# Kernel optimization log

Measured on AMD Instinct MI355X. Metric: run time of the kernel, lower is better.

## Reference

```python
import jax, jax.numpy as jnp
import numpy as np

B, S, D = 4, 2048, 1024
H = 16
HD = D // H  # head_dim = 64


def setup_inputs() -> dict:
    key = jax.random.key(0)
    ks = jax.random.split(key, 5)
    scale = 1.0 / np.sqrt(D)
    return {
        "sequence_features": jax.random.normal(ks[0], (B, S, D), dtype=jnp.float32),
        "Wq": jax.random.normal(ks[1], (D, D), dtype=jnp.float32) * scale,
        "bq": jnp.zeros((D,), dtype=jnp.float32),
        "Wk": jax.random.normal(ks[2], (D, D), dtype=jnp.float32) * scale,
        "bk": jnp.zeros((D,), dtype=jnp.float32),
        "Wv": jax.random.normal(ks[3], (D, D), dtype=jnp.float32) * scale,
        "bv": jnp.zeros((D,), dtype=jnp.float32),
        "Wo": jax.random.normal(ks[4], (D, D), dtype=jnp.float32) * scale,
        "bo": jnp.zeros((D,), dtype=jnp.float32),
    }


def reference(sequence_features, Wq, bq, Wk, bk, Wv, bv, Wo, bo):
    x = sequence_features  # [B, S, D]
    # projections (torch Linear: x @ W.T + b; here W stored as [D_in, D_out])
    Q = x @ Wq + bq
    K = x @ Wk + bk
    V = x @ Wv + bv
    # split heads -> [B, H, S, HD]
    def heads(t):
        return t.reshape(B, S, H, HD).transpose(0, 2, 1, 3)
    Qh, Kh, Vh = heads(Q), heads(K), heads(V)
    # scaled dot-product attention (no mask, dropout off / eval mode)
    energy = jnp.einsum("bhqd,bhkd->bhqk", Qh, Kh) / jnp.sqrt(jnp.float32(HD))
    attn = jax.nn.softmax(energy, axis=-1)
    ctx = jnp.einsum("bhqk,bhkd->bhqd", attn, Vh)  # [B, H, S, HD]
    ctx = ctx.transpose(0, 2, 1, 3).reshape(B, S, D)
    out = ctx @ Wo + bo  # [B, S, D]
    return out.mean(axis=1)  # context vector [B, D]
```

## Files before the change

kernel.cpp:

```cpp
#include <hip/hip_runtime.h>
#include <hip/hip_bf16.h>

#define NB 4
#define NS 2048
#define ND 1024
#define NH 16

typedef __attribute__((ext_vector_type(8))) short short8;
typedef __attribute__((ext_vector_type(4))) float f32x4;

__device__ __forceinline__ unsigned short f2b(float f) {
  unsigned int u = __float_as_uint(f);
  u = (u + 0x7fffu + ((u >> 16) & 1u)) >> 16;
  return (unsigned short)u;
}
__device__ __forceinline__ unsigned int pkbf(float a, float b) {
  return (unsigned int)f2b(a) | ((unsigned int)f2b(b) << 16);
}
__device__ __forceinline__ void gload16(const void* g, void* l) {
  __builtin_amdgcn_global_load_lds(
      (const __attribute__((address_space(1))) unsigned int*)g,
      (__attribute__((address_space(3))) unsigned int*)l, 16, 0, 0);
}
__device__ __forceinline__ int sw2(int row) { return (row ^ (row >> 2)) & 3; }

__global__ void conv_x(const float* __restrict__ x, unsigned short* __restrict__ xb) {
  int i = blockIdx.x * 256 + threadIdx.x;
  float4 v = ((const float4*)x)[i];
  ushort4 o;
  o.x = f2b(v.x); o.y = f2b(v.y); o.z = f2b(v.z); o.w = f2b(v.w);
  ((ushort4*)xb)[i] = o;
}

__global__ void conv_wt(const float* __restrict__ Wq, const float* __restrict__ Wk,
                        const float* __restrict__ Wv, unsigned short* __restrict__ Wtq,
                        unsigned short* __restrict__ Wtk, unsigned short* __restrict__ Wtv) {
  const int z = blockIdx.z;
  const float* W = (z == 0) ? Wq : (z == 1) ? Wk : Wv;
  unsigned short* Wt = (z == 0) ? Wtq : (z == 1) ? Wtk : Wtv;
  __shared__ float t[32][33];
  const int tid = threadIdx.x;
  const int row = tid >> 3, c4 = (tid & 7) * 4;
  float4 v = *(const float4*)(W + (size_t)(blockIdx.y * 32 + row) * ND + blockIdx.x * 32 + c4);
  t[row][c4] = v.x; t[row][c4 + 1] = v.y; t[row][c4 + 2] = v.z; t[row][c4 + 3] = v.w;
  __syncthreads();
  ushort4 o;
  o.x = f2b(t[c4][row]); o.y = f2b(t[c4 + 1][row]);
  o.z = f2b(t[c4 + 2][row]); o.w = f2b(t[c4 + 3][row]);
  *(ushort4*)(Wt + (size_t)(blockIdx.x * 32 + row) * ND + blockIdx.y * 32 + c4) = o;
}

__global__ __launch_bounds__(256) void qkv_gemm(
    const unsigned short* __restrict__ xb,
    const unsigned short* __restrict__ Wtq, const unsigned short* __restrict__ Wtk,
    const unsigned short* __restrict__ Wtv,
    const float* __restrict__ bq, const float* __restrict__ bk, const float* __restrict__ bv,
    unsigned short* __restrict__ Qb, unsigned short* __restrict__ Kb,
    unsigned short* __restrict__ Vt) {
  const int z = blockIdx.z;
  const unsigned short* Wt = (z == 0) ? Wtq : (z == 1) ? Wtk : Wtv;
  const float* bias = (z == 0) ? bq : (z == 1) ? bk : bv;
  const int tn = blockIdx.x, tm = blockIdx.y;
  __shared__ __align__(16) unsigned short Al[2][128 * 32];
  __shared__ __align__(16) unsigned short Bl[2][128 * 32];
  const int tid = threadIdx.x;
  const int lane = tid & 63, w = tid >> 6;
  const int c = lane & 15, g = lane >> 4;
  const int mo = (w >> 1) * 64, no = (w & 1) * 64;

  f32x4 acc[4][4];
#pragma unroll
  for (int i = 0; i < 4; i++)
#pragma unroll
    for (int j = 0; j < 4; j++) acc[i][j] = (f32x4){0.f, 0.f, 0.f, 0.f};

  const int r0 = tid >> 2, g0 = tid & 3;
  const int r1 = (256 + tid) >> 2, g1 = (256 + tid) & 3;
  const unsigned short* gA0 = xb + (size_t)(tm * 128 + r0) * ND + (g0 ^ sw2(r0)) * 8;
  const unsigned short* gA1 = xb + (size_t)(tm * 128 + r1) * ND + (g1 ^ sw2(r1)) * 8;
  const unsigned short* gB0 = Wt + (size_t)(tn * 128 + r0) * ND + (g0 ^ sw2(r0)) * 8;
  const unsigned short* gB1 = Wt + (size_t)(tn * 128 + r1) * ND + (g1 ^ sw2(r1)) * 8;
  const int lo0 = w * 512, lo1 = 2048 + w * 512;

  gload16(gA0, &Al[0][lo0]); gload16(gA1, &Al[0][lo1]);
  gload16(gB0, &Bl[0][lo0]); gload16(gB1, &Bl[0][lo1]);
  __syncthreads();

  for (int kk = 0; kk < 32; ++kk) {
    const int cur = kk & 1;
    if (kk < 31) {
      const int ko = (kk + 1) * 32;
      gload16(gA0 + ko, &Al[cur ^ 1][lo0]); gload16(gA1 + ko, &Al[cur ^ 1][lo1]);
      gload16(gB0 + ko, &Bl[cur ^ 1][lo0]); gload16(gB1 + ko, &Bl[cur ^ 1][lo1]);
    }
    short8 af[4], bf[4];
#pragma unroll
    for (int i = 0; i < 4; i++) {
      int row = mo + i * 16 + c;
      af[i] = *(const short8*)&Al[cur][row * 32 + (g ^ sw2(row)) * 8];
    }
#pragma unroll
    for (int j = 0; j < 4; j++) {
      int row = no + j * 16 + c;
      bf[j] = *(const short8*)&Bl[cur][row * 32 + (g ^ sw2(row)) * 8];
    }
#pragma unroll
    for (int i = 0; i < 4; i++)
#pragma unroll
      for (int j = 0; j < 4; j++)
        acc[i][j] = __builtin_amdgcn_mfma_f32_16x16x32_bf16(af[i], bf[j], acc[i][j], 0, 0, 0);
    __syncthreads();
  }

  if (z < 2) {
    unsigned short* Out = (z == 0) ? Qb : Kb;
    const float sc = (z == 0) ? 0.125f : 1.0f;
#pragma unroll
    for (int j = 0; j < 4; j++) {
      int col = tn * 128 + no + j * 16 + c;
      float bv_ = bias[col];
#pragma unroll
      for (int i = 0; i < 4; i++) {
        int rowb = tm * 128 + mo + i * 16 + 4 * g;
#pragma unroll
        for (int r = 0; r < 4; r++) {
          float v = (acc[i][j][r] + bv_) * sc;
          float vn = __shfl_xor(v, 1, 64);
          if (!(lane & 1))
            *(unsigned int*)(Out + (size_t)(rowb + r) * ND + col) = pkbf(v, vn);
        }
      }
    }
  } else {
#pragma unroll
    for (int j = 0; j < 4; j++) {
      int col = tn * 128 + no + j * 16 + c;
      float bv_ = bias[col];
      int h = col >> 6, hd = col & 63;
#pragma unroll
      for (int i = 0; i < 4; i++) {
        int rowg = tm * 128 + mo + i * 16 + 4 * g;
        int bi = rowg >> 11, s = rowg & 2047;
        uint2 u;
        u.x = pkbf(acc[i][j][0] + bv_, acc[i][j][1] + bv_);
        u.y = pkbf(acc[i][j][2] + bv_, acc[i][j][3] + bv_);
        *(uint2*)(Vt + ((size_t)((bi * NH + h) * 64 + hd) * NS + s)) = u;
      }
    }
  }
}

__global__ __launch_bounds__(256) void attn_kernel(
    const unsigned short* __restrict__ Qb, const unsigned short* __restrict__ Kb,
    const unsigned short* __restrict__ Vt, float* __restrict__ mean_ctx) {
  const int qt = blockIdx.x, h = blockIdx.y, b = blockIdx.z;
  const int tid = threadIdx.x, lane = tid & 63, w = tid >> 6;
  const int c = lane & 15, g = lane >> 4;
  __shared__ __align__(16) unsigned short Klds[2][32 * 64];
  __shared__ __align__(16) unsigned short Vlds[2][64 * 32];
  __shared__ float redl[4][64];

  const int qg = qt * 64 + w * 16 + c;
  const unsigned short* qbase = Qb + (size_t)(b * NS + qg) * ND + h * 64 + g * 8;
  const short8 qf0 = *(const short8*)(qbase);
  const short8 qf1 = *(const short8*)(qbase + 32);

  const int krow = tid >> 3, kg = tid & 7;
  const unsigned short* gK = Kb + (size_t)(b * NS + krow) * ND + h * 64 + ((kg ^ (krow & 7)) * 8);
  const int vd = tid >> 2, vg = tid & 3;
  const unsigned short* gV = Vt + (size_t)((b * NH + h) * 64 + vd) * NS + ((vg ^ sw2(vd)) * 8);

  f32x4 accc[4];
#pragma unroll
  for (int nt = 0; nt < 4; nt++) accc[nt] = (f32x4){0.f, 0.f, 0.f, 0.f};
  float m_run = -1e30f, l_run = 0.f;

  gload16(gK, &Klds[0][w * 512]);
  gload16(gV, &Vlds[0][w * 512]);
  __syncthreads();

  for (int kc = 0; kc < 64; ++kc) {
    const int cur = kc & 1;
    if (kc < 63) {
      gload16(gK + (size_t)(kc + 1) * 32 * ND, &Klds[cur ^ 1][w * 512]);
      gload16(gV + (kc + 1) * 32, &Vlds[cur ^ 1][w * 512]);
    }
    f32x4 accE[2];
#pragma unroll
    for (int mt = 0; mt < 2; ++mt) {
      int row = mt * 16 + c;
      short8 k0 = *(const short8*)&Klds[cur][row * 64 + ((g ^ (row & 7)) * 8)];
      short8 k1 = *(const short8*)&Klds[cur][row * 64 + (((g + 4) ^ (row & 7)) * 8)];
      f32x4 zz = (f32x4){0.f, 0.f, 0.f, 0.f};
      accE[mt] = __builtin_amdgcn_mfma_f32_16x16x32_bf16(k0, qf0, zz, 0, 0, 0);
      accE[mt] = __builtin_amdgcn_mfma_f32_16x16x32_bf16(k1, qf1, accE[mt], 0, 0, 0);
    }
    float cm = fmaxf(fmaxf(fmaxf(accE[0][0], accE[0][1]), fmaxf(accE[0][2], accE[0][3])),
                     fmaxf(fmaxf(accE[1][0], accE[1][1]), fmaxf(accE[1][2], accE[1][3])));
    cm = fmaxf(cm, __shfl_xor(cm, 16, 64));
    cm = fmaxf(cm, __shfl_xor(cm, 32, 64));
    float mnew = fmaxf(m_run, cm);
    float sf = __expf(m_run - mnew);
    float p[8];
#pragma unroll
    for (int r = 0; r < 4; r++) {
      p[r] = __expf(accE[0][r] - mnew);
      p[4 + r] = __expf(accE[1][r] - mnew);
    }
    float cs = ((p[0] + p[1]) + (p[2] + p[3])) + ((p[4] + p[5]) + (p[6] + p[7]));
    cs += __shfl_xor(cs, 16, 64);
    cs += __shfl_xor(cs, 32, 64);
    l_run = l_run * sf + cs;
    m_run = mnew;
    float sf0 = __shfl(sf, 4 * g + 0, 64), sf1 = __shfl(sf, 4 * g + 1, 64);
    float sf2 = __shfl(sf, 4 * g + 2, 64), sf3 = __shfl(sf, 4 * g + 3, 64);
#pragma unroll
    for (int nt = 0; nt < 4; nt++) {
      accc[nt][0] *= sf0; accc[nt][1] *= sf1; accc[nt][2] *= sf2; accc[nt][3] *= sf3;
    }
    unsigned int pk0 = pkbf(p[0], p[1]), pk1 = pkbf(p[2], p[3]);
    unsigned int pk2 = pkbf(p[4], p[5]), pk3 = pkbf(p[6], p[7]);
    int srcA = (g & 1) * 32 + c, srcB = srcA + 16;
    unsigned int a0 = (unsigned int)__shfl((int)pk0, srcA, 64);
    unsigned int h0 = (unsigned int)__shfl((int)pk2, srcA, 64);
    unsigned int a1 = (unsigned int)__shfl((int)pk1, srcA, 64);
    unsigned int h1 = (unsigned int)__shfl((int)pk3, srcA, 64);
    unsigned int a2 = (unsigned int)__shfl((int)pk0, srcB, 64);
    unsigned int h2 = (unsigned int)__shfl((int)pk2, srcB, 64);
    unsigned int a3 = (unsigned int)__shfl((int)pk1, srcB, 64);
    unsigned int h3 = (unsigned int)__shfl((int)pk3, srcB, 64);
    union { unsigned int u[4]; short8 v; } pf;
    pf.u[0] = (g < 2) ? a0 : h0;
    pf.u[1] = (g < 2) ? a1 : h1;
    pf.u[2] = (g < 2) ? a2 : h2;
    pf.u[3] = (g < 2) ? a3 : h3;
#pragma unroll
    for (int nt = 0; nt < 4; nt++) {
      int d = nt * 16 + c;
      short8 vf = *(const short8*)&Vlds[cur][d * 32 + ((g ^ sw2(d)) * 8)];
      accc[nt] = __builtin_amdgcn_mfma_f32_16x16x32_bf16(pf.v, vf, accc[nt], 0, 0, 0);
    }
    __syncthreads();
  }

  float i0 = 1.f / __shfl(l_run, 4 * g + 0, 64);
  float i1 = 1.f / __shfl(l_run, 4 * g + 1, 64);
  float i2 = 1.f / __shfl(l_run, 4 * g + 2, 64);
  float i3 = 1.f / __shfl(l_run, 4 * g + 3, 64);
#pragma unroll
  for (int nt = 0; nt < 4; nt++) {
    float s = accc[nt][0] * i0 + accc[nt][1] * i1 + accc[nt][2] * i2 + accc[nt][3] * i3;
    s += __shfl_xor(s, 16, 64);
    s += __shfl_xor(s, 32, 64);
    if (g == 0) redl[w][nt * 16 + c] = s;
  }
  __syncthreads();
  if (tid < 64) {
    float tot = redl[0][tid] + redl[1][tid] + redl[2][tid] + redl[3][tid];
    atomicAdd(&mean_ctx[(size_t)b * ND + h * 64 + tid], tot * (1.0f / (float)NS));
  }
}

__global__ void out_proj(const float* __restrict__ mc, const float* __restrict__ Wo,
                         const float* __restrict__ bo, float* __restrict__ out) {
  const int b = blockIdx.y;
  const int d = blockIdx.x * 256 + threadIdx.x;
  const float* m = mc + (size_t)b * ND;
  float acc = bo[d];
#pragma unroll 8
  for (int k = 0; k < ND; ++k) acc = fmaf(m[k], Wo[(size_t)k * ND + d], acc);
  out[(size_t)b * ND + d] = acc;
}

extern "C" void kernel_launch(void* const* d_in, const int* in_sizes, int n_in,
                              void* d_out, int out_size, void* d_ws, size_t ws_size,
                              hipStream_t stream) {
  const float* x  = (const float*)d_in[0];
  const float* Wq = (const float*)d_in[1];
  const float* bq = (const float*)d_in[2];
  const float* Wk = (const float*)d_in[3];
  const float* bk = (const float*)d_in[4];
  const float* Wv = (const float*)d_in[5];
  const float* bv = (const float*)d_in[6];
  const float* Wo = (const float*)d_in[7];
  const float* bo = (const float*)d_in[8];
  float* out = (float*)d_out;

  char* ws = (char*)d_ws;
  size_t off = 0;
  unsigned short* xb  = (unsigned short*)(ws + off); off += (size_t)NB * NS * ND * 2;
  unsigned short* Wtq = (unsigned short*)(ws + off); off += (size_t)ND * ND * 2;
  unsigned short* Wtk = (unsigned short*)(ws + off); off += (size_t)ND * ND * 2;
  unsigned short* Wtv = (unsigned short*)(ws + off); off += (size_t)ND * ND * 2;
  unsigned short* Qb  = (unsigned short*)(ws + off); off += (size_t)NB * NS * ND * 2;
  unsigned short* Kb  = (unsigned short*)(ws + off); off += (size_t)NB * NS * ND * 2;
  unsigned short* Vt  = (unsigned short*)(ws + off); off += (size_t)NB * NS * ND * 2;
  float* mctx = (float*)(ws + off); off += (size_t)NB * ND * 4;

  hipMemsetAsync(mctx, 0, (size_t)NB * ND * 4, stream);
  conv_x<<<(NB * NS * ND / 4) / 256, 256, 0, stream>>>(x, xb);
  conv_wt<<<dim3(32, 32, 3), 256, 0, stream>>>(Wq, Wk, Wv, Wtq, Wtk, Wtv);
  qkv_gemm<<<dim3(ND / 128, NB * NS / 128, 3), 256, 0, stream>>>(
      xb, Wtq, Wtk, Wtv, bq, bk, bv, Qb, Kb, Vt);
  attn_kernel<<<dim3(NS / 64, NH, NB), 256, 0, stream>>>(Qb, Kb, Vt, mctx);
  out_proj<<<dim3(ND / 256, NB), 256, 0, stream>>>(mctx, Wo, bo, out);
}
```

Measured before the change: 437.2 us.

## Rewrite attention with 32x32 MFMA, 256-query tiles, lazy rescale, deterministic reduce

The attention kernel now processes 256 queries per block (64 per wave, in two 32-row groups) using 32x32x16 bf16 MFMA, with 64-key K/V chunks double-buffered in LDS. Softmax skips rescaling unless the max grows by more than a threshold, uses hardware cvt_pk_bf16 and permlane32_swap to form P operands, and raises wave priority around MFMA sections. Per-tile partial means are written to a buffer and summed by a new reduce kernel instead of atomics and a memset. This cuts K/V reloads per query and shuffle overhead, but adds register pressure and yields 4x fewer blocks (512), which may hurt occupancy.

Result: faster. 403.1 us (-7.8%).

```diff
diff --git a/kernel.cpp b/kernel.cpp
--- a/kernel.cpp
+++ b/kernel.cpp
@@ -8,6 +8,8 @@
 
 typedef __attribute__((ext_vector_type(8))) short short8;
 typedef __attribute__((ext_vector_type(4))) float f32x4;
+typedef __attribute__((ext_vector_type(16))) float f32x16;
+typedef __attribute__((ext_vector_type(2))) int v2i;
 
 __device__ __forceinline__ unsigned short f2b(float f) {
   unsigned int u = __float_as_uint(f);
@@ -16,6 +18,14 @@
 }
 __device__ __forceinline__ unsigned int pkbf(float a, float b) {
   return (unsigned int)f2b(a) | ((unsigned int)f2b(b) << 16);
+}
+__device__ __forceinline__ unsigned int cvtpk(float lo, float hi) {
+  unsigned int r;
+  asm("v_cvt_pk_bf16_f32 %0, %1, %2" : "=v"(r) : "v"(lo), "v"(hi));
+  return r;
+}
+__device__ __forceinline__ v2i plswap(unsigned int a, unsigned int b) {
+  return __builtin_amdgcn_permlane32_swap((int)a, (int)b, false, false);
 }
 __device__ __forceinline__ void gload16(const void* g, void* l) {
   __builtin_amdgcn_global_load_lds(
@@ -150,115 +160,166 @@
   }
 }
 
+__device__ __forceinline__ void softmax_pack(const f32x16& e, float& m, float& l,
+                                             f32x16& c0, f32x16& c1, int hi,
+                                             short8* pa) {
+  float pm = e[0];
+#pragma unroll
+  for (int r = 1; r < 16; r++) pm = fmaxf(pm, e[r]);
+  pm = fmaxf(pm, __shfl_xor(pm, 32, 64));
+  if (__any(pm > m + 8.f)) {
+    float mn = fmaxf(m, pm);
+    float sf = __expf(m - mn);
+#pragma unroll
+    for (int r = 0; r < 16; r++) {
+      int qlr = (r & 3) + 8 * (r >> 2) + 4 * hi;
+      float sr = __shfl(sf, qlr, 64);
+      c0[r] *= sr; c1[r] *= sr;
+    }
+    l *= sf; m = mn;
+  }
+  float p[16];
+#pragma unroll
+  for (int r = 0; r < 16; r++) p[r] = __expf(e[r] - m);
+  float cs = 0.f;
+#pragma unroll
+  for (int r = 0; r < 16; r++) cs += p[r];
+  cs += __shfl_xor(cs, 32, 64);
+  l += cs;
+  unsigned int u0[4], u1[4];
+#pragma unroll
+  for (int mq = 0; mq < 4; mq++) {
+    u0[mq] = cvtpk(p[4 * mq], p[4 * mq + 1]);
+    u1[mq] = cvtpk(p[4 * mq + 2], p[4 * mq + 3]);
+  }
+#pragma unroll
+  for (int si = 0; si < 2; si++) {
+    v2i a = plswap(u0[2 * si], u0[2 * si + 1]);
+    v2i bb = plswap(u1[2 * si], u1[2 * si + 1]);
+    union { unsigned int u[4]; short8 v; } pf;
+    pf.u[0] = (unsigned int)a[0];
+    pf.u[1] = (unsigned int)bb[0];
+    pf.u[2] = (unsigned int)a[1];
+    pf.u[3] = (unsigned int)bb[1];
+    pa[si] = pf.v;
+  }
+}
+
 __global__ __launch_bounds__(256) void attn_kernel(
     const unsigned short* __restrict__ Qb, const unsigned short* __restrict__ Kb,
-    const unsigned short* __restrict__ Vt, float* __restrict__ mean_ctx) {
+    const unsigned short* __restrict__ Vt, float* __restrict__ mean_part) {
   const int qt = blockIdx.x, h = blockIdx.y, b = blockIdx.z;
   const int tid = threadIdx.x, lane = tid & 63, w = tid >> 6;
-  const int c = lane & 15, g = lane >> 4;
-  __shared__ __align__(16) unsigned short Klds[2][32 * 64];
-  __shared__ __align__(16) unsigned short Vlds[2][64 * 32];
+  const int ql_ = lane & 31, hi = lane >> 5;
+
+  __shared__ __align__(16) unsigned short Kl[2][64 * 64];
+  __shared__ __align__(16) unsigned short Vl[2][64 * 64];
   __shared__ float redl[4][64];
 
-  const int qg = qt * 64 + w * 16 + c;
-  const unsigned short* qbase = Qb + (size_t)(b * NS + qg) * ND + h * 64 + g * 8;
-  const short8 qf0 = *(const short8*)(qbase);
-  const short8 qf1 = *(const short8*)(qbase + 32);
-
-  const int krow = tid >> 3, kg = tid & 7;
-  const unsigned short* gK = Kb + (size_t)(b * NS + krow) * ND + h * 64 + ((kg ^ (krow & 7)) * 8);
-  const int vd = tid >> 2, vg = tid & 3;
-  const unsigned short* gV = Vt + (size_t)((b * NH + h) * 64 + vd) * NS + ((vg ^ sw2(vd)) * 8);
-
-  f32x4 accc[4];
-#pragma unroll
-  for (int nt = 0; nt < 4; nt++) accc[nt] = (f32x4){0.f, 0.f, 0.f, 0.f};
-  float m_run = -1e30f, l_run = 0.f;
-
-  gload16(gK, &Klds[0][w * 512]);
-  gload16(gV, &Vlds[0][w * 512]);
+  short8 qf[2][4];
+#pragma unroll
+  for (int qg = 0; qg < 2; qg++) {
+    const unsigned short* qb =
+        Qb + ((size_t)b * NS + qt * 256 + w * 64 + qg * 32 + ql_) * ND + h * 64 + 8 * hi;
+#pragma unroll
+    for (int s = 0; s < 4; s++) qf[qg][s] = *(const short8*)(qb + 16 * s);
+  }
+
+  const int rid = tid >> 3, gcol = tid & 7;
+  const int gsw = (gcol ^ (rid & 7)) * 8;
+  const unsigned short* gK0 = Kb + ((size_t)b * NS + rid) * ND + h * 64 + gsw;
+  const unsigned short* gK1 = gK0 + (size_t)32 * ND;
+  const unsigned short* gV0 = Vt + ((size_t)(b * NH + h) * 64 + rid) * NS + gsw;
+  const unsigned short* gV1 = gV0 + (size_t)32 * NS;
+
+#define STAGE_KV(buf, kc)                                              \
+  {                                                                    \
+    const size_t ko = (size_t)(kc) * 64;                               \
+    gload16(gK0 + ko * ND, &Kl[buf][w * 512]);                         \
+    gload16(gK1 + ko * ND, &Kl[buf][2048 + w * 512]);                  \
+    gload16(gV0 + ko, &Vl[buf][w * 512]);                              \
+    gload16(gV1 + ko, &Vl[buf][2048 + w * 512]);                       \
+  }
+
+  const f32x16 Z16 = {0.f, 0.f, 0.f, 0.f, 0.f, 0.f, 0.f, 0.f,
+                      0.f, 0.f, 0.f, 0.f, 0.f, 0.f, 0.f, 0.f};
+  f32x16 ctx00 = Z16, ctx01 = Z16, ctx10 = Z16, ctx11 = Z16;
+  float m0 = -1e30f, m1 = -1e30f, l0 = 0.f, l1 = 0.f;
+
+  STAGE_KV(0, 0);
   __syncthreads();
 
-  for (int kc = 0; kc < 64; ++kc) {
+  for (int kc = 0; kc < 32; ++kc) {
     const int cur = kc & 1;
-    if (kc < 63) {
-      gload16(gK + (size_t)(kc + 1) * 32 * ND, &Klds[cur ^ 1][w * 512]);
-      gload16(gV + (kc + 1) * 32, &Vlds[cur ^ 1][w * 512]);
-    }
-    f32x4 accE[2];
-#pragma unroll
-    for (int mt = 0; mt < 2; ++mt) {
-      int row = mt * 16 + c;
-      short8 k0 = *(const short8*)&Klds[cur][row * 64 + ((g ^ (row & 7)) * 8)];
-      short8 k1 = *(const short8*)&Klds[cur][row * 64 + (((g + 4) ^ (row & 7)) * 8)];
-      f32x4 zz = (f32x4){0.f, 0.f, 0.f, 0.f};
-      accE[mt] = __builtin_amdgcn_mfma_f32_16x16x32_bf16(k0, qf0, zz, 0, 0, 0);
-      accE[mt] = __builtin_amdgcn_mfma_f32_16x16x32_bf16(k1, qf1, accE[mt], 0, 0, 0);
-    }
-    float cm = fmaxf(fmaxf(fmaxf(accE[0][0], accE[0][1]), fmaxf(accE[0][2], accE[0][3])),
-                     fmaxf(fmaxf(accE[1][0], accE[1][1]), fmaxf(accE[1][2], accE[1][3])));
-    cm = fmaxf(cm, __shfl_xor(cm, 16, 64));
-    cm = fmaxf(cm, __shfl_xor(cm, 32, 64));
-    float mnew = fmaxf(m_run, cm);
-    float sf = __expf(m_run - mnew);
-    float p[8];
-#pragma unroll
-    for (int r = 0; r < 4; r++) {
-      p[r] = __expf(accE[0][r] - mnew);
-      p[4 + r] = __expf(accE[1][r] - mnew);
-    }
-    float cs = ((p[0] + p[1]) + (p[2] + p[3])) + ((p[4] + p[5]) + (p[6] + p[7]));
-    cs += __shfl_xor(cs, 16, 64);
-    cs += __shfl_xor(cs, 32, 64);
-    l_run = l_run * sf + cs;
-    m_run = mnew;
-    float sf0 = __shfl(sf, 4 * g + 0, 64), sf1 = __shfl(sf, 4 * g + 1, 64);
-    float sf2 = __shfl(sf, 4 * g + 2, 64), sf3 = __shfl(sf, 4 * g + 3, 64);
-#pragma unroll
-    for (int nt = 0; nt < 4; nt++) {
-      accc[nt][0] *= sf0; accc[nt][1] *= sf1; accc[nt][2] *= sf2; accc[nt][3] *= sf3;
-    }
-    unsigned int pk0 = pkbf(p[0], p[1]), pk1 = pkbf(p[2], p[3]);
-    unsigned int pk2 = pkbf(p[4], p[5]), pk3 = pkbf(p[6], p[7]);
-    int srcA = (g & 1) * 32 + c, srcB = srcA + 16;
-    unsigned int a0 = (unsigned int)__shfl((int)pk0, srcA, 64);
-    unsigned int h0 = (unsigned int)__shfl((int)pk2, srcA, 64);
-    unsigned int a1 = (unsigned int)__shfl((int)pk1, srcA, 64);
-    unsigned int h1 = (unsigned int)__shfl((int)pk3, srcA, 64);
-    unsigned int a2 = (unsigned int)__shfl((int)pk0, srcB, 64);
-    unsigned int h2 = (unsigned int)__shfl((int)pk2, srcB, 64);
-    unsigned int a3 = (unsigned int)__shfl((int)pk1, srcB, 64);
-    unsigned int h3 = (unsigned int)__shfl((int)pk3, srcB, 64);
-    union { unsigned int u[4]; short8 v; } pf;
-    pf.u[0] = (g < 2) ? a0 : h0;
-    pf.u[1] = (g < 2) ? a1 : h1;
-    pf.u[2] = (g < 2) ? a2 : h2;
-    pf.u[3] = (g < 2) ? a3 : h3;
-#pragma unroll
-    for (int nt = 0; nt < 4; nt++) {
-      int d = nt * 16 + c;
-      short8 vf = *(const short8*)&Vlds[cur][d * 32 + ((g ^ sw2(d)) * 8)];
-      accc[nt] = __builtin_amdgcn_mfma_f32_16x16x32_bf16(pf.v, vf, accc[nt], 0, 0, 0);
+    if (kc < 31) STAGE_KV(cur ^ 1, kc + 1);
+#pragma unroll
+    for (int kg = 0; kg < 2; kg++) {
+      short8 kf[4];
+#pragma unroll
+      for (int s = 0; s < 4; s++)
+        kf[s] = *(const short8*)&Kl[cur][(kg * 32 + ql_) * 64 +
+                                         (((2 * s + hi) ^ (ql_ & 7)) * 8)];
+      __builtin_amdgcn_s_setprio(1);
+      f32x16 e0 = __builtin_amdgcn_mfma_f32_32x32x16_bf16(kf[0], qf[0][0], Z16, 0, 0, 0);
+      f32x16 e1 = __builtin_amdgcn_mfma_f32_32x32x16_bf16(kf[0], qf[1][0], Z16, 0, 0, 0);
+#pragma unroll
+      for (int s = 1; s < 4; s++) {
+        e0 = __builtin_amdgcn_mfma_f32_32x32x16_bf16(kf[s], qf[0][s], e0, 0, 0, 0);
+        e1 = __builtin_amdgcn_mfma_f32_32x32x16_bf16(kf[s], qf[1][s], e1, 0, 0, 0);
+      }
+      __builtin_amdgcn_s_setprio(0);
+
+      short8 pa0[2], pa1[2];
+      softmax_pack(e0, m0, l0, ctx00, ctx01, hi, pa0);
+      softmax_pack(e1, m1, l1, ctx10, ctx11, hi, pa1);
+
+      __builtin_amdgcn_s_setprio(1);
+#pragma unroll
+      for (int si = 0; si < 2; si++) {
+#pragma unroll
+        for (int dg = 0; dg < 2; dg++) {
+          short8 vf = *(const short8*)&Vl[cur][(dg * 32 + ql_) * 64 +
+                        (((4 * kg + 2 * si + hi) ^ (ql_ & 7)) * 8)];
+          if (dg == 0) {
+            ctx00 = __builtin_amdgcn_mfma_f32_32x32x16_bf16(pa0[si], vf, ctx00, 0, 0, 0);
+            ctx10 = __builtin_amdgcn_mfma_f32_32x32x16_bf16(pa1[si], vf, ctx10, 0, 0, 0);
+          } else {
+            ctx01 = __builtin_amdgcn_mfma_f32_32x32x16_bf16(pa0[si], vf, ctx01, 0, 0, 0);
+            ctx11 = __builtin_amdgcn_mfma_f32_32x32x16_bf16(pa1[si], vf, ctx11, 0, 0, 0);
+          }
+        }
+      }
+      __builtin_amdgcn_s_setprio(0);
     }
     __syncthreads();
   }
 
-  float i0 = 1.f / __shfl(l_run, 4 * g + 0, 64);
-  float i1 = 1.f / __shfl(l_run, 4 * g + 1, 64);
-  float i2 = 1.f / __shfl(l_run, 4 * g + 2, 64);
-  float i3 = 1.f / __shfl(l_run, 4 * g + 3, 64);
-#pragma unroll
-  for (int nt = 0; nt < 4; nt++) {
-    float s = accc[nt][0] * i0 + accc[nt][1] * i1 + accc[nt][2] * i2 + accc[nt][3] * i3;
-    s += __shfl_xor(s, 16, 64);
-    s += __shfl_xor(s, 32, 64);
-    if (g == 0) redl[w][nt * 16 + c] = s;
-  }
+  float linv0 = 1.f / l0, linv1 = 1.f / l1;
+  float s0 = 0.f, s1 = 0.f;
+#pragma unroll
+  for (int r = 0; r < 16; r++) {
+    int qlr = (r & 3) + 8 * (r >> 2) + 4 * hi;
+    float lv0 = __shfl(linv0, qlr, 64);
+    float lv1 = __shfl(linv1, qlr, 64);
+    s0 += ctx00[r] * lv0 + ctx10[r] * lv1;
+    s1 += ctx01[r] * lv0 + ctx11[r] * lv1;
+  }
+  s0 += __shfl_xor(s0, 32, 64);
+  s1 += __shfl_xor(s1, 32, 64);
+  if (lane < 32) { redl[w][lane] = s0; redl[w][32 + lane] = s1; }
   __syncthreads();
   if (tid < 64) {
     float tot = redl[0][tid] + redl[1][tid] + redl[2][tid] + redl[3][tid];
-    atomicAdd(&mean_ctx[(size_t)b * ND + h * 64 + tid], tot * (1.0f / (float)NS));
-  }
+    mean_part[((size_t)qt * NB + b) * ND + h * 64 + tid] = tot * (1.0f / (float)NS);
+  }
+}
+
+__global__ void reduce_mctx(const float* __restrict__ mp, float* __restrict__ mctx) {
+  int i = blockIdx.x * 256 + threadIdx.x;
+  float s = 0.f;
+#pragma unroll
+  for (int q = 0; q < NS / 256; ++q) s += mp[(size_t)q * NB * ND + i];
+  mctx[i] = s;
 }
 
 __global__ void out_proj(const float* __restrict__ mc, const float* __restrict__ Wo,
@@ -295,13 +356,14 @@
   unsigned short* Qb  = (unsigned short*)(ws + off); off += (size_t)NB * NS * ND * 2;
   unsigned short* Kb  = (unsigned short*)(ws + off); off += (size_t)NB * NS * ND * 2;
   unsigned short* Vt  = (unsigned short*)(ws + off); off += (size_t)NB * NS * ND * 2;
-  float* mctx = (float*)(ws + off); off += (size_t)NB * ND * 4;
-
-  hipMemsetAsync(mctx, 0, (size_t)NB * ND * 4, stream);
+  float* mpart = (float*)(ws + off); off += (size_t)(NS / 256) * NB * ND * 4;
+  float* mctx  = (float*)(ws + off); off += (size_t)NB * ND * 4;
+
   conv_x<<<(NB * NS * ND / 4) / 256, 256, 0, stream>>>(x, xb);
   conv_wt<<<dim3(32, 32, 3), 256, 0, stream>>>(Wq, Wk, Wv, Wtq, Wtk, Wtv);
   qkv_gemm<<<dim3(ND / 128, NB * NS / 128, 3), 256, 0, stream>>>(
       xb, Wtq, Wtk, Wtv, bq, bk, bv, Qb, Kb, Vt);
-  attn_kernel<<<dim3(NS / 64, NH, NB), 256, 0, stream>>>(Qb, Kb, Vt, mctx);
+  attn_kernel<<<dim3(NS / 256, NH, NB), 256, 0, stream>>>(Qb, Kb, Vt, mpart);
+  reduce_mctx<<<(NB * ND) / 256, 256, 0, stream>>>(mpart, mctx);
   out_proj<<<dim3(ND / 256, NB), 256, 0, stream>>>(mctx, Wo, bo, out);
 }
```
